# Kernel tuning notes

Measured on AMD Instinct MI355X. Metric: run time of the kernel, lower is better.

Reference implementation:

```python
import jax, jax.numpy as jnp
import numpy as np

D_MODEL = 2048
NUM_HEADS = 16
NUM_KV_HEADS = 4
HEAD_DIM = D_MODEL // NUM_HEADS
ROPE_THETA = 10000.0


def setup_inputs() -> dict:
    key = jax.random.key(0)
    ks = jax.random.split(key, 5)
    B, S = 2, 2048
    scale = 0.02
    return {
        "x": jax.random.normal(ks[0], (B, S, D_MODEL), dtype=jnp.float32),
        "wq": jax.random.normal(ks[1], (D_MODEL, NUM_HEADS * HEAD_DIM), dtype=jnp.float32) * scale,
        "wk": jax.random.normal(ks[2], (D_MODEL, NUM_KV_HEADS * HEAD_DIM), dtype=jnp.float32) * scale,
        "wv": jax.random.normal(ks[3], (D_MODEL, NUM_KV_HEADS * HEAD_DIM), dtype=jnp.float32) * scale,
        "wo": jax.random.normal(ks[4], (NUM_HEADS * HEAD_DIM, D_MODEL), dtype=jnp.float32) * scale,
    }


def _rope_cos_sin(seq_len, head_dim, dtype):
    # Llama-style: freqs over even indices, angles = pos * inv_freq
    inv_freq = 1.0 / (ROPE_THETA ** (jnp.arange(0, head_dim, 2, dtype=jnp.float32) / head_dim))
    ang = jnp.arange(seq_len, dtype=jnp.float32)[:, None] * inv_freq[None, :]  # [S, hd/2]
    cos = jnp.cos(ang).astype(dtype)[None, :, None, :]  # [1,S,1,hd/2]
    sin = jnp.sin(ang).astype(dtype)[None, :, None, :]
    return cos, sin


def _apply_rope(x, cos, sin):
    # x: [B,S,H,hd]; interleaved complex rotation on pairs (x[2i], x[2i+1])
    x1 = x[..., 0::2]
    x2 = x[..., 1::2]
    y1 = x1 * cos - x2 * sin
    y2 = x1 * sin + x2 * cos
    return jnp.stack([y1, y2], axis=-1).reshape(x.shape)


def reference(x, wq, wk, wv, wo):
    B, S, D = x.shape
    H, KV, hd = NUM_HEADS, NUM_KV_HEADS, HEAD_DIM
    g = H // KV
    q = (x @ wq).reshape(B, S, H, hd)
    k = (x @ wk).reshape(B, S, KV, hd)
    v = (x @ wv).reshape(B, S, KV, hd)
    cos, sin = _rope_cos_sin(S, hd, x.dtype)
    q = _apply_rope(q, cos, sin)
    k = _apply_rope(k, cos, sin)
    q = q.transpose(0, 2, 1, 3)  # [B,H,S,hd]
    k = k.transpose(0, 2, 1, 3)  # [B,KV,S,hd]
    v = v.transpose(0, 2, 1, 3)
    k = jnp.repeat(k, g, axis=1)  # GQA: [B,H,S,hd]
    v = jnp.repeat(v, g, axis=1)
    attn = jnp.einsum('bqsh,bqlh->bqsl', q, k) * (1.0 / np.sqrt(hd)).astype(np.float32)
    attn = jax.nn.softmax(attn, axis=-1)  # non-causal, as in source
    out = jnp.einsum('bqsl,bqlh->bqsh', attn, v)
    out = out.transpose(0, 2, 1, 3).reshape(B, S, D)
    return out @ wo
```

## Files before the change

### kernel.cpp

```cpp
#include <hip/hip_runtime.h>


typedef __attribute__((ext_vector_type(8))) short short8;
typedef __attribute__((ext_vector_type(4))) float f32x4;

#define DEV static __device__ __forceinline__

#define NB 2
#define NS 2048
#define ND 2048
#define NH 16
#define NKV 4
#define HD 128
#define NQKV 3072

DEV unsigned short f2bf(float f) {
  union { float f; unsigned u; } v; v.f = f;
  unsigned r = v.u + 0x7fffu + ((v.u >> 16) & 1u);
  return (unsigned short)(r >> 16);
}
DEV float bf2f(unsigned short u) {
  union { unsigned u; float f; } v; v.u = ((unsigned)u) << 16; return v.f;
}
DEV unsigned pack2bf_rne(float a, float b) {
  return (unsigned)f2bf(a) | ((unsigned)f2bf(b) << 16);
}
DEV unsigned cvtpk(float a, float b) {
  unsigned r;
  asm("v_cvt_pk_bf16_f32 %0, %1, %2" : "=v"(r) : "v"(a), "v"(b));
  return r;
}

DEV void swap32(unsigned &x, unsigned &y) {
  asm volatile("v_permlane32_swap_b32 %0, %1" : "+v"(x), "+v"(y));
}
DEV void swap16(unsigned &x, unsigned &y) {
  asm volatile("v_permlane16_swap_b32 %0, %1" : "+v"(x), "+v"(y));
}

typedef const __attribute__((address_space(1))) void* gas1_t;
typedef __attribute__((address_space(3))) void* las3_t;
DEV void gload16(const void* g, void* l) {
  __builtin_amdgcn_global_load_lds((gas1_t)g, (las3_t)l, 16, 0, 0);
}

DEV f32x4 mfma16(short8 a, short8 b, f32x4 c) {
  return __builtin_amdgcn_mfma_f32_16x16x32_bf16(a, b, c, 0, 0, 0);
}


__global__ __launch_bounds__(256) void convert_x_kernel(const float* __restrict__ x,
                                                        unsigned short* __restrict__ xb) {
  size_t i = ((size_t)blockIdx.x * 256 + threadIdx.x) * 4;
  float4 v = *(const float4*)(x + i);
  unsigned long long pack = (unsigned long long)f2bf(v.x)
                          | ((unsigned long long)f2bf(v.y) << 16)
                          | ((unsigned long long)f2bf(v.z) << 32)
                          | ((unsigned long long)f2bf(v.w) << 48);
  *(unsigned long long*)(xb + i) = pack;
}

__global__ __launch_bounds__(256) void transpose_w_kernel(const float* __restrict__ src,
                                                          unsigned short* __restrict__ dst,
                                                          int K, int N) {
  __shared__ float tile[64][65];
  const int k0 = blockIdx.x * 64, n0 = blockIdx.y * 64;
  for (int i = threadIdx.x; i < 1024; i += 256) {
    int r = i >> 4, c4 = (i & 15) * 4;
    float4 v = *(const float4*)&src[(size_t)(k0 + r) * N + n0 + c4];
    tile[r][c4] = v.x; tile[r][c4 + 1] = v.y; tile[r][c4 + 2] = v.z; tile[r][c4 + 3] = v.w;
  }
  __syncthreads();
  for (int i = threadIdx.x; i < 1024; i += 256) {
    int rn = i >> 4, k4 = (i & 15) * 4;
    ushort4 o;
    o.x = f2bf(tile[k4][rn]);     o.y = f2bf(tile[k4 + 1][rn]);
    o.z = f2bf(tile[k4 + 2][rn]); o.w = f2bf(tile[k4 + 3][rn]);
    *(ushort4*)&dst[(size_t)(n0 + rn) * K + k0 + k4] = o;
  }
}

__global__ __launch_bounds__(256) void rope_table_kernel(float2* __restrict__ tab) {
  int t = blockIdx.x * 256 + threadIdx.x;
  int s = t >> 6, i = t & 63;
  float freq = powf(10000.0f, -(float)i * (1.0f / 64.0f));
  float ang = (float)s * freq;
  tab[t] = make_float2(cosf(ang), sinf(ang));
}

__global__ __launch_bounds__(256) void rope_scatter_kernel(const unsigned short* __restrict__ QKV,
                                                           const float2* __restrict__ tab,
                                                           unsigned short* __restrict__ Qb,
                                                           unsigned short* __restrict__ Kb) {
  int t = blockIdx.x * 256 + threadIdx.x;
  const float qscale = 0.12751741161895452f;
  if (t < (1 << 22)) {
    int i = t & 63, h = (t >> 6) & 15, s = (t >> 10) & 2047, b = t >> 21;
    const unsigned short* p = QKV + (size_t)(b * NS + s) * NQKV + h * HD + 2 * i;
    float2 cs = tab[s * 64 + i];
    float x1 = bf2f(p[0]), x2 = bf2f(p[1]);
    unsigned short* q = Qb + (size_t)((b * NH + h) * NS + s) * HD + 2 * i;
    q[0] = f2bf((x1 * cs.x - x2 * cs.y) * qscale);
    q[1] = f2bf((x1 * cs.y + x2 * cs.x) * qscale);
  } else {
    int u = t - (1 << 22);
    int i = u & 63, kv = (u >> 6) & 3, s = (u >> 8) & 2047, b = u >> 19;
    const unsigned short* p = QKV + (size_t)(b * NS + s) * NQKV + 2048 + kv * HD + 2 * i;
    float2 cs = tab[s * 64 + i];
    float x1 = bf2f(p[0]), x2 = bf2f(p[1]);
    unsigned short* k = Kb + (size_t)((b * NKV + kv) * NS + s) * HD + 2 * i;
    k[0] = f2bf(x1 * cs.x - x2 * cs.y);
    k[1] = f2bf(x1 * cs.y + x2 * cs.x);
  }
}

__global__ __launch_bounds__(256) void transpose_v_kernel(const unsigned short* __restrict__ QKV,
                                                          unsigned short* __restrict__ Vt) {
  __shared__ unsigned short tile[64][65];
  const int bk = blockIdx.x, b = bk >> 2, kv = bk & 3;
  const int s0 = blockIdx.y * 64, d0 = blockIdx.z * 64;
  for (int i = threadIdx.x; i < 4096; i += 256) {
    int r = i >> 6, c = i & 63;
    tile[r][c] = QKV[(size_t)(b * NS + s0 + r) * NQKV + 2560 + kv * HD + d0 + c];
  }
  __syncthreads();
  for (int i = threadIdx.x; i < 4096; i += 256) {
    int r = i >> 6, c = i & 63;
    Vt[(size_t)((b * NKV + kv) * HD + d0 + r) * NS + s0 + c] = tile[c][r];
  }
}


template <int N, bool OUTBF16>
__global__ __launch_bounds__(512) void gemm256_kernel(const unsigned short* __restrict__ A,
                                                      const unsigned short* __restrict__ Bt,
                                                      void* __restrict__ Cout) {
  __shared__ unsigned short Sm[2][2][2][256 * 32];
  const int K = 2048, NT = K / 64;
  const int tid = threadIdx.x, wid = tid >> 6, lane = tid & 63;
  const int wm = wid >> 2, wn = wid & 3;

  const int nwg = gridDim.x * gridDim.y;
  const int bid = blockIdx.y * gridDim.x + blockIdx.x;
  const int swzb = (bid & 7) * (nwg >> 3) + (bid >> 3);
  const int m0 = (swzb % gridDim.x) * 256;
  const int n0 = (swzb / gridDim.x) * 256;

  const int cl = lane & 15, g = lane >> 4;
  const int rsw = (cl & 3) << 3;

  const int stg_row = tid >> 2;
  const int stg_colE = ((tid & 3) * 8) ^ ((stg_row & 3) << 3);
  const unsigned short* Abase = A + (size_t)(m0 + stg_row) * K + stg_colE;
  const unsigned short* Bbase = Bt + (size_t)(n0 + stg_row) * K + stg_colE;

  auto stage_half = [&](int buf, int kt, int h) {
    const int op = h & 1, kh = h >> 1;
    const unsigned short* s0 = (op ? Bbase : Abase) + kt + kh * 32;
    unsigned short* dst = &Sm[buf][op][kh][wid * 512];
    gload16(s0, dst);
    gload16(s0 + (size_t)128 * K, dst + 4096);
  };

  auto read_a = [&](int buf, int kh, int r) -> short8 {
    const int row = wm * 128 + r * 16 + cl;
    return *(const short8*)&Sm[buf][0][kh][row * 32 + ((g * 8) ^ rsw)];
  };
  auto read_b = [&](int buf, int kh, int cf) -> short8 {
    const int row = wn * 64 + cf * 16 + cl;
    return *(const short8*)&Sm[buf][1][kh][row * 32 + ((g * 8) ^ rsw)];
  };

  f32x4 acc[8][4] = {};
  short8 af[8];

#pragma unroll
  for (int h = 0; h < 4; ++h) stage_half(0, 0, h);

  for (int t = 0; t < NT - 1; ++t) {
    const int buf = t & 1, ktn = (t + 1) * 64;
#pragma unroll
    for (int ph = 0; ph < 4; ++ph) {
      stage_half(buf ^ 1, ktn, ph);
      asm volatile("s_waitcnt vmcnt(6)" ::: "memory");
      __builtin_amdgcn_s_barrier();
      const int kh = ph >> 1, ch = ph & 1;
      if (ch == 0) {
#pragma unroll
        for (int r = 0; r < 8; ++r) af[r] = read_a(buf, kh, r);
      }
      short8 b0 = read_b(buf, kh, ch * 2);
      short8 b1 = read_b(buf, kh, ch * 2 + 1);
      __builtin_amdgcn_s_setprio(1);
#pragma unroll
      for (int r = 0; r < 8; ++r) {
        acc[r][ch * 2]     = mfma16(af[r], b0, acc[r][ch * 2]);
        acc[r][ch * 2 + 1] = mfma16(af[r], b1, acc[r][ch * 2 + 1]);
      }
      __builtin_amdgcn_s_setprio(0);
      __builtin_amdgcn_s_barrier();
    }
  }

  asm volatile("s_waitcnt vmcnt(0)" ::: "memory");
  __builtin_amdgcn_s_barrier();
  {
    const int buf = (NT - 1) & 1;
#pragma unroll
    for (int kh = 0; kh < 2; ++kh) {
#pragma unroll
      for (int r = 0; r < 8; ++r) af[r] = read_a(buf, kh, r);
#pragma unroll
      for (int cf = 0; cf < 4; ++cf) {
        short8 b = read_b(buf, kh, cf);
#pragma unroll
        for (int r = 0; r < 8; ++r) acc[r][cf] = mfma16(af[r], b, acc[r][cf]);
      }
    }
  }

  if (OUTBF16) {
    unsigned short* C = (unsigned short*)Cout;
#pragma unroll
    for (int r = 0; r < 8; ++r) {
      const int row0 = m0 + wm * 128 + r * 16 + g * 4;
#pragma unroll
      for (int cf = 0; cf < 4; ++cf) {
        const int col = n0 + wn * 64 + cf * 16 + cl;
#pragma unroll
        for (int j = 0; j < 4; ++j)
          C[(size_t)(row0 + j) * N + col] = f2bf(acc[r][cf][j]);
      }
    }
  } else {
    float* C = (float*)Cout;
#pragma unroll
    for (int r = 0; r < 8; ++r) {
      const int row0 = m0 + wm * 128 + r * 16 + g * 4;
#pragma unroll
      for (int cf = 0; cf < 4; ++cf) {
        const int col = n0 + wn * 64 + cf * 16 + cl;
#pragma unroll
        for (int j = 0; j < 4; ++j)
          C[(size_t)(row0 + j) * N + col] = acc[r][cf][j];
      }
    }
  }
}


__global__ __launch_bounds__(256, 2) void attn_kernel(const unsigned short* __restrict__ Qb,
                                                      const unsigned short* __restrict__ Kb,
                                                      const unsigned short* __restrict__ Vt,
                                                      unsigned short* __restrict__ O) {
  __shared__ unsigned short Ks[2][64 * 128];
  __shared__ unsigned short Vs[2][128 * 64];
  const int tid = threadIdx.x, wid = tid >> 6, lane = tid & 63;
  const int blk = blockIdx.x;
  const int qt = blk & 15, h = (blk >> 4) & 15, b = blk >> 8;
  const int kvh = h >> 2;
  const int q0 = qt * 128 + wid * 32;

  const unsigned short* qhead = Qb + (size_t)((b * NH + h) * NS) * HD;
  const unsigned short* khead = Kb + (size_t)((b * NKV + kvh) * NS) * HD;
  const unsigned short* vhead = Vt + (size_t)((b * NKV + kvh) * HD) * NS;

  const int cl = lane & 15, g4 = (lane >> 4) * 4, hi8 = (lane >> 4) * 8;
  const int swk = (lane & 7) << 3;

  auto stageKV = [&](int buf, int kt) {
#pragma unroll
    for (int i = 0; i < 4; ++i) {
      int row = i * 16 + (tid >> 4);
      int col = ((tid & 15) * 8) ^ ((row & 7) << 3);
      gload16(khead + (size_t)(kt + row) * HD + col, &Ks[buf][i * 2048 + wid * 512]);
    }
#pragma unroll
    for (int i = 0; i < 4; ++i) {
      int row = i * 32 + (tid >> 3);
      int col = ((tid & 7) * 8) ^ ((row & 7) << 3);
      gload16(vhead + (size_t)row * NS + kt + col, &Vs[buf][i * 2048 + wid * 512]);
    }
  };

  stageKV(0, 0);

  short8 qf[2][4];
#pragma unroll
  for (int r = 0; r < 2; ++r)
#pragma unroll
    for (int kk = 0; kk < 4; ++kk)
      qf[r][kk] = *(const short8*)(qhead + (size_t)(q0 + r * 16 + cl) * HD + kk * 32 + hi8);

  f32x4 od[2][8] = {};
  float mrun[2] = {-1e30f, -1e30f}, lpart[2] = {0.f, 0.f};

  int cur = 0;
  for (int it = 0; it < NS / 64; ++it) {
    if (it + 1 < NS / 64) {
      stageKV(cur ^ 1, (it + 1) * 64);
      asm volatile("s_waitcnt vmcnt(8)" ::: "memory");
    } else {
      asm volatile("s_waitcnt vmcnt(0)" ::: "memory");
    }
    __builtin_amdgcn_s_barrier();

    const unsigned short* ks = Ks[cur];
    const unsigned short* vs = Vs[cur];

    f32x4 s[2][4];
#pragma unroll
    for (int r = 0; r < 2; ++r)
#pragma unroll
      for (int c4 = 0; c4 < 4; ++c4) s[r][c4] = f32x4{0.f, 0.f, 0.f, 0.f};
    __builtin_amdgcn_s_setprio(1);
#pragma unroll
    for (int c4 = 0; c4 < 4; ++c4)
#pragma unroll
      for (int kk = 0; kk < 4; ++kk) {
        short8 kf = *(const short8*)&ks[((c4 * 16 + cl) * 128 + kk * 32 + hi8) ^ swk];
        s[0][c4] = mfma16(kf, qf[0][kk], s[0][c4]);
        s[1][c4] = mfma16(kf, qf[1][kk], s[1][c4]);
      }
    __builtin_amdgcn_s_setprio(0);

    float mt[2];
#pragma unroll
    for (int r = 0; r < 2; ++r) {
      float m = fmaxf(fmaxf(fmaxf(s[r][0][0], s[r][0][1]), fmaxf(s[r][0][2], s[r][0][3])),
                      fmaxf(fmaxf(s[r][1][0], s[r][1][1]), fmaxf(s[r][1][2], s[r][1][3])));
      float m2 = fmaxf(fmaxf(fmaxf(s[r][2][0], s[r][2][1]), fmaxf(s[r][2][2], s[r][2][3])),
                       fmaxf(fmaxf(s[r][3][0], s[r][3][1]), fmaxf(s[r][3][2], s[r][3][3])));
      m = fmaxf(m, m2);
      m = fmaxf(m, __shfl_xor(m, 16, 64));
      m = fmaxf(m, __shfl_xor(m, 32, 64));
      mt[r] = m;
    }
    bool need = (mt[0] > mrun[0] + 8.0f) || (mt[1] > mrun[1] + 8.0f);
    if (__any(need)) {
#pragma unroll
      for (int r = 0; r < 2; ++r) {
        float mn = fmaxf(mrun[r], mt[r]);
        float corr = __builtin_amdgcn_exp2f(mrun[r] - mn);
        mrun[r] = mn;
        lpart[r] *= corr;
#pragma unroll
        for (int c = 0; c < 8; ++c)
          od[r][c] *= corr;
      }
    }
#pragma unroll
    for (int r = 0; r < 2; ++r) {
      float acc = 0.f;
#pragma unroll
      for (int c4 = 0; c4 < 4; ++c4)
#pragma unroll
        for (int j = 0; j < 4; ++j) {
          float p = __builtin_amdgcn_exp2f(s[r][c4][j] - mrun[r]);
          s[r][c4][j] = p;
          acc += p;
        }
      lpart[r] += acc;
    }

    short8 pb[2][2];
#pragma unroll
    for (int r = 0; r < 2; ++r) {
      unsigned w00 = cvtpk(s[r][0][0], s[r][0][1]), w01 = cvtpk(s[r][0][2], s[r][0][3]);
      unsigned w10 = cvtpk(s[r][1][0], s[r][1][1]), w11 = cvtpk(s[r][1][2], s[r][1][3]);
      unsigned w20 = cvtpk(s[r][2][0], s[r][2][1]), w21 = cvtpk(s[r][2][2], s[r][2][3]);
      unsigned w30 = cvtpk(s[r][3][0], s[r][3][1]), w31 = cvtpk(s[r][3][2], s[r][3][3]);
      union { unsigned u[4]; short8 v; } t0, t1;
      swap32(w00, w10); swap16(w00, w10); t0.u[0] = w00; t0.u[2] = w10;
      swap32(w01, w11); swap16(w01, w11); t0.u[1] = w01; t0.u[3] = w11;
      swap32(w20, w30); swap16(w20, w30); t1.u[0] = w20; t1.u[2] = w30;
      swap32(w21, w31); swap16(w21, w31); t1.u[1] = w21; t1.u[3] = w31;
      pb[r][0] = t0.v;
      pb[r][1] = t1.v;
    }

    __builtin_amdgcn_s_setprio(1);
#pragma unroll
    for (int c = 0; c < 8; ++c) {
      const int rr = c * 16 + cl;
      short8 vf0 = *(const short8*)&vs[(rr * 64 + hi8) ^ swk];
      short8 vf1 = *(const short8*)&vs[(rr * 64 + 32 + hi8) ^ swk];
      od[0][c] = mfma16(vf0, pb[0][0], od[0][c]);
      od[0][c] = mfma16(vf1, pb[0][1], od[0][c]);
      od[1][c] = mfma16(vf0, pb[1][0], od[1][c]);
      od[1][c] = mfma16(vf1, pb[1][1], od[1][c]);
    }
    __builtin_amdgcn_s_setprio(0);
    __builtin_amdgcn_s_barrier();
    cur ^= 1;
  }

  float linv[2];
#pragma unroll
  for (int r = 0; r < 2; ++r) {
    float l = lpart[r];
    l += __shfl_xor(l, 16, 64);
    l += __shfl_xor(l, 32, 64);
    linv[r] = 1.0f / l;
  }
#pragma unroll
  for (int r = 0; r < 2; ++r) {
    const size_t row = (size_t)(b * NS + q0 + 16 * r + cl);
#pragma unroll
    for (int c = 0; c < 8; ++c) {
      uint2 pk;
      pk.x = pack2bf_rne(od[r][c][0] * linv[r], od[r][c][1] * linv[r]);
      pk.y = pack2bf_rne(od[r][c][2] * linv[r], od[r][c][3] * linv[r]);
      *(uint2*)(O + row * ND + h * HD + c * 16 + g4) = pk;
    }
  }
}


extern "C" void kernel_launch(void* const* d_in, const int* in_sizes, int n_in,
                              void* d_out, int out_size, void* d_ws, size_t ws_size,
                              hipStream_t stream) {
  const float* x  = (const float*)d_in[0];
  const float* wq = (const float*)d_in[1];
  const float* wk = (const float*)d_in[2];
  const float* wv = (const float*)d_in[3];
  const float* wo = (const float*)d_in[4];
  float* out = (float*)d_out;
  char* ws = (char*)d_ws;

  unsigned short* xb   = (unsigned short*)(ws + 0);
  unsigned short* wT   = (unsigned short*)(ws + 16777216);
  unsigned short* woT  = (unsigned short*)(ws + 29360128);
  float2*         tab  = (float2*)(ws + 37748736);
  unsigned short* QKV  = (unsigned short*)(ws + 38797312);
  unsigned short* Qb   = xb;
  unsigned short* Kb   = wT;
  unsigned short* Vt   = (unsigned short*)(ws + 16777216 + 4194304);
  unsigned short* Obuf = QKV;

  convert_x_kernel<<<8192, 256, 0, stream>>>(x, xb);
  transpose_w_kernel<<<dim3(32, 32), 256, 0, stream>>>(wq, wT, 2048, 2048);
  transpose_w_kernel<<<dim3(32, 8),  256, 0, stream>>>(wk, wT + (size_t)2048 * 2048, 2048, 512);
  transpose_w_kernel<<<dim3(32, 8),  256, 0, stream>>>(wv, wT + (size_t)2560 * 2048, 2048, 512);
  transpose_w_kernel<<<dim3(32, 32), 256, 0, stream>>>(wo, woT, 2048, 2048);
  rope_table_kernel<<<512, 256, 0, stream>>>(tab);

  gemm256_kernel<NQKV, true><<<dim3(16, 12), 512, 0, stream>>>(xb, wT, QKV);

  rope_scatter_kernel<<<20480, 256, 0, stream>>>(QKV, tab, Qb, Kb);
  transpose_v_kernel<<<dim3(8, 32, 2), 256, 0, stream>>>(QKV, Vt);

  attn_kernel<<<512, 256, 0, stream>>>(Qb, Kb, Vt, Obuf);

  gemm256_kernel<ND, false><<<dim3(16, 8), 512, 0, stream>>>(Obuf, woT, out);
}
```

Baseline: 243.4 us.

## Fuse weight-prep launches and use 128-row tiles for output projection GEMM

The four weight-transpose launches and the rope-table launch are merged into one prep kernel that picks its work from blockIdx.y, which removes launch overhead and lets the small jobs run concurrently. The GEMM is templated on the M tile height. The output projection now uses BM=128, which doubles the grid from 128 to 256 workgroups so all CUs on the MI355X get work. The vmcnt waits are adjusted because the A operand now issues one load per stage instead of two. The smaller tiles lower per-block arithmetic intensity and increase redundant loads of B.

```diff
diff --git a/kernel.cpp b/kernel.cpp
--- a/kernel.cpp
+++ b/kernel.cpp
@@ -60,11 +60,31 @@
   *(unsigned long long*)(xb + i) = pack;
 }
 
-__global__ __launch_bounds__(256) void transpose_w_kernel(const float* __restrict__ src,
-                                                          unsigned short* __restrict__ dst,
-                                                          int K, int N) {
+__global__ __launch_bounds__(256) void prep_fused_kernel(const float* __restrict__ wq,
+                                                         const float* __restrict__ wk,
+                                                         const float* __restrict__ wv,
+                                                         const float* __restrict__ wo,
+                                                         unsigned short* __restrict__ wT,
+                                                         unsigned short* __restrict__ woT,
+                                                         float2* __restrict__ tab) {
+  const int ty = blockIdx.y;
+  if (ty >= 80) {
+    int t = ((ty - 80) * 32 + blockIdx.x) * 256 + threadIdx.x;
+    int s = t >> 6, i = t & 63;
+    float freq = powf(10000.0f, -(float)i * (1.0f / 64.0f));
+    float ang = (float)s * freq;
+    tab[t] = make_float2(cosf(ang), sinf(ang));
+    return;
+  }
+  const float* src;
+  unsigned short* dst;
+  int N, n0;
+  if (ty < 32)      { src = wq; dst = wT;                         N = 2048; n0 = ty * 64; }
+  else if (ty < 40) { src = wk; dst = wT + (size_t)2048 * 2048;   N = 512;  n0 = (ty - 32) * 64; }
+  else if (ty < 48) { src = wv; dst = wT + (size_t)2560 * 2048;   N = 512;  n0 = (ty - 40) * 64; }
+  else              { src = wo; dst = woT;                        N = 2048; n0 = (ty - 48) * 64; }
+  const int K = 2048, k0 = blockIdx.x * 64;
   __shared__ float tile[64][65];
-  const int k0 = blockIdx.x * 64, n0 = blockIdx.y * 64;
   for (int i = threadIdx.x; i < 1024; i += 256) {
     int r = i >> 4, c4 = (i & 15) * 4;
     float4 v = *(const float4*)&src[(size_t)(k0 + r) * N + n0 + c4];
@@ -78,14 +98,6 @@
     o.z = f2bf(tile[k4 + 2][rn]); o.w = f2bf(tile[k4 + 3][rn]);
     *(ushort4*)&dst[(size_t)(n0 + rn) * K + k0 + k4] = o;
   }
-}
-
-__global__ __launch_bounds__(256) void rope_table_kernel(float2* __restrict__ tab) {
-  int t = blockIdx.x * 256 + threadIdx.x;
-  int s = t >> 6, i = t & 63;
-  float freq = powf(10000.0f, -(float)i * (1.0f / 64.0f));
-  float ang = (float)s * freq;
-  tab[t] = make_float2(cosf(ang), sinf(ang));
 }
 
 __global__ __launch_bounds__(256) void rope_scatter_kernel(const unsigned short* __restrict__ QKV,
@@ -131,19 +143,21 @@
 }
 
 
-template <int N, bool OUTBF16>
+template <int N, int BM, bool OUTBF16>
 __global__ __launch_bounds__(512) void gemm256_kernel(const unsigned short* __restrict__ A,
                                                       const unsigned short* __restrict__ Bt,
                                                       void* __restrict__ Cout) {
-  __shared__ unsigned short Sm[2][2][2][256 * 32];
+  __shared__ unsigned short SmA[2][2][BM * 32];
+  __shared__ unsigned short SmB[2][2][256 * 32];
   const int K = 2048, NT = K / 64;
+  constexpr int RF = BM / 32;
   const int tid = threadIdx.x, wid = tid >> 6, lane = tid & 63;
   const int wm = wid >> 2, wn = wid & 3;
 
   const int nwg = gridDim.x * gridDim.y;
   const int bid = blockIdx.y * gridDim.x + blockIdx.x;
   const int swzb = (bid & 7) * (nwg >> 3) + (bid >> 3);
-  const int m0 = (swzb % gridDim.x) * 256;
+  const int m0 = (swzb % gridDim.x) * BM;
   const int n0 = (swzb / gridDim.x) * 256;
 
   const int cl = lane & 15, g = lane >> 4;
@@ -156,23 +170,30 @@
 
   auto stage_half = [&](int buf, int kt, int h) {
     const int op = h & 1, kh = h >> 1;
-    const unsigned short* s0 = (op ? Bbase : Abase) + kt + kh * 32;
-    unsigned short* dst = &Sm[buf][op][kh][wid * 512];
-    gload16(s0, dst);
-    gload16(s0 + (size_t)128 * K, dst + 4096);
+    if (op == 0) {
+      const unsigned short* s0 = Abase + kt + kh * 32;
+      unsigned short* dst = &SmA[buf][kh][wid * 512];
+      gload16(s0, dst);
+      if constexpr (BM == 256) gload16(s0 + (size_t)128 * K, dst + 4096);
+    } else {
+      const unsigned short* s0 = Bbase + kt + kh * 32;
+      unsigned short* dst = &SmB[buf][kh][wid * 512];
+      gload16(s0, dst);
+      gload16(s0 + (size_t)128 * K, dst + 4096);
+    }
   };
 
   auto read_a = [&](int buf, int kh, int r) -> short8 {
-    const int row = wm * 128 + r * 16 + cl;
-    return *(const short8*)&Sm[buf][0][kh][row * 32 + ((g * 8) ^ rsw)];
+    const int row = wm * (BM / 2) + r * 16 + cl;
+    return *(const short8*)&SmA[buf][kh][row * 32 + ((g * 8) ^ rsw)];
   };
   auto read_b = [&](int buf, int kh, int cf) -> short8 {
     const int row = wn * 64 + cf * 16 + cl;
-    return *(const short8*)&Sm[buf][1][kh][row * 32 + ((g * 8) ^ rsw)];
+    return *(const short8*)&SmB[buf][kh][row * 32 + ((g * 8) ^ rsw)];
   };
 
-  f32x4 acc[8][4] = {};
-  short8 af[8];
+  f32x4 acc[RF][4] = {};
+  short8 af[RF];
 
 #pragma unroll
   for (int h = 0; h < 4; ++h) stage_half(0, 0, h);
@@ -182,18 +203,23 @@
 #pragma unroll
     for (int ph = 0; ph < 4; ++ph) {
       stage_half(buf ^ 1, ktn, ph);
-      asm volatile("s_waitcnt vmcnt(6)" ::: "memory");
+      if constexpr (BM == 256) {
+        asm volatile("s_waitcnt vmcnt(6)" ::: "memory");
+      } else {
+        if (ph & 1) asm volatile("s_waitcnt vmcnt(6)" ::: "memory");
+        else        asm volatile("s_waitcnt vmcnt(4)" ::: "memory");
+      }
       __builtin_amdgcn_s_barrier();
       const int kh = ph >> 1, ch = ph & 1;
       if (ch == 0) {
 #pragma unroll
-        for (int r = 0; r < 8; ++r) af[r] = read_a(buf, kh, r);
+        for (int r = 0; r < RF; ++r) af[r] = read_a(buf, kh, r);
       }
       short8 b0 = read_b(buf, kh, ch * 2);
       short8 b1 = read_b(buf, kh, ch * 2 + 1);
       __builtin_amdgcn_s_setprio(1);
 #pragma unroll
-      for (int r = 0; r < 8; ++r) {
+      for (int r = 0; r < RF; ++r) {
         acc[r][ch * 2]     = mfma16(af[r], b0, acc[r][ch * 2]);
         acc[r][ch * 2 + 1] = mfma16(af[r], b1, acc[r][ch * 2 + 1]);
       }
@@ -209,12 +235,12 @@
 #pragma unroll
     for (int kh = 0; kh < 2; ++kh) {
 #pragma unroll
-      for (int r = 0; r < 8; ++r) af[r] = read_a(buf, kh, r);
+      for (int r = 0; r < RF; ++r) af[r] = read_a(buf, kh, r);
 #pragma unroll
       for (int cf = 0; cf < 4; ++cf) {
         short8 b = read_b(buf, kh, cf);
 #pragma unroll
-        for (int r = 0; r < 8; ++r) acc[r][cf] = mfma16(af[r], b, acc[r][cf]);
+        for (int r = 0; r < RF; ++r) acc[r][cf] = mfma16(af[r], b, acc[r][cf]);
       }
     }
   }
@@ -222,8 +248,8 @@
   if (OUTBF16) {
     unsigned short* C = (unsigned short*)Cout;
 #pragma unroll
-    for (int r = 0; r < 8; ++r) {
-      const int row0 = m0 + wm * 128 + r * 16 + g * 4;
+    for (int r = 0; r < RF; ++r) {
+      const int row0 = m0 + wm * (BM / 2) + r * 16 + g * 4;
 #pragma unroll
       for (int cf = 0; cf < 4; ++cf) {
         const int col = n0 + wn * 64 + cf * 16 + cl;
@@ -235,8 +261,8 @@
   } else {
     float* C = (float*)Cout;
 #pragma unroll
-    for (int r = 0; r < 8; ++r) {
-      const int row0 = m0 + wm * 128 + r * 16 + g * 4;
+    for (int r = 0; r < RF; ++r) {
+      const int row0 = m0 + wm * (BM / 2) + r * 16 + g * 4;
 #pragma unroll
       for (int cf = 0; cf < 4; ++cf) {
         const int col = n0 + wn * 64 + cf * 16 + cl;
@@ -439,18 +465,14 @@
   unsigned short* Obuf = QKV;
 
   convert_x_kernel<<<8192, 256, 0, stream>>>(x, xb);
-  transpose_w_kernel<<<dim3(32, 32), 256, 0, stream>>>(wq, wT, 2048, 2048);
-  transpose_w_kernel<<<dim3(32, 8),  256, 0, stream>>>(wk, wT + (size_t)2048 * 2048, 2048, 512);
-  transpose_w_kernel<<<dim3(32, 8),  256, 0, stream>>>(wv, wT + (size_t)2560 * 2048, 2048, 512);
-  transpose_w_kernel<<<dim3(32, 32), 256, 0, stream>>>(wo, woT, 2048, 2048);
-  rope_table_kernel<<<512, 256, 0, stream>>>(tab);
-
-  gemm256_kernel<NQKV, true><<<dim3(16, 12), 512, 0, stream>>>(xb, wT, QKV);
+  prep_fused_kernel<<<dim3(32, 96), 256, 0, stream>>>(wq, wk, wv, wo, wT, woT, tab);
+
+  gemm256_kernel<NQKV, 256, true><<<dim3(16, 12), 512, 0, stream>>>(xb, wT, QKV);
 
   rope_scatter_kernel<<<20480, 256, 0, stream>>>(QKV, tab, Qb, Kb);
   transpose_v_kernel<<<dim3(8, 32, 2), 256, 0, stream>>>(QKV, Vt);
 
   attn_kernel<<<512, 256, 0, stream>>>(Qb, Kb, Vt, Obuf);
 
-  gemm256_kernel<ND, false><<<dim3(16, 8), 512, 0, stream>>>(Obuf, woT, out);
-}
+  gemm256_kernel<ND, 128, false><<<dim3(32, 8), 512, 0, stream>>>(Obuf, woT, out);
+}
```

Result: slower. 263.3 us (+8.1%).

## Fuse prep kernels, scatter QKV in GEMM epilogue, load V directly in attention

Applied to the files above, without the earlier changes.

Merges the four weight transposes and the rope table into one launch. The QKV GEMM epilogue now writes Q and K straight into head-major layout and V pre-transposed, so the separate scatter and V-transpose passes go away. RoPE is applied in place with 16-byte vector loads and stores. The attention kernel stops staging V through LDS and reads V fragments from global memory into registers each iteration, which adds register pressure and uncoalesced global reads in exchange for less LDS use and a barrier-free pipeline.

```diff
diff --git a/kernel.cpp b/kernel.cpp
--- a/kernel.cpp
+++ b/kernel.cpp
@@ -60,11 +60,31 @@
   *(unsigned long long*)(xb + i) = pack;
 }
 
-__global__ __launch_bounds__(256) void transpose_w_kernel(const float* __restrict__ src,
-                                                          unsigned short* __restrict__ dst,
-                                                          int K, int N) {
+__global__ __launch_bounds__(256) void prep_fused_kernel(const float* __restrict__ wq,
+                                                         const float* __restrict__ wk,
+                                                         const float* __restrict__ wv,
+                                                         const float* __restrict__ wo,
+                                                         unsigned short* __restrict__ wT,
+                                                         unsigned short* __restrict__ woT,
+                                                         float2* __restrict__ tab) {
+  const int ty = blockIdx.y;
+  if (ty >= 80) {
+    int t = ((ty - 80) * 32 + blockIdx.x) * 256 + threadIdx.x;
+    int s = t >> 6, i = t & 63;
+    float freq = powf(10000.0f, -(float)i * (1.0f / 64.0f));
+    float ang = (float)s * freq;
+    tab[t] = make_float2(cosf(ang), sinf(ang));
+    return;
+  }
+  const float* src;
+  unsigned short* dst;
+  int N, n0;
+  if (ty < 32)      { src = wq; dst = wT;                         N = 2048; n0 = ty * 64; }
+  else if (ty < 40) { src = wk; dst = wT + (size_t)2048 * 2048;   N = 512;  n0 = (ty - 32) * 64; }
+  else if (ty < 48) { src = wv; dst = wT + (size_t)2560 * 2048;   N = 512;  n0 = (ty - 40) * 64; }
+  else              { src = wo; dst = woT;                        N = 2048; n0 = (ty - 48) * 64; }
+  const int K = 2048, k0 = blockIdx.x * 64;
   __shared__ float tile[64][65];
-  const int k0 = blockIdx.x * 64, n0 = blockIdx.y * 64;
   for (int i = threadIdx.x; i < 1024; i += 256) {
     int r = i >> 4, c4 = (i & 15) * 4;
     float4 v = *(const float4*)&src[(size_t)(k0 + r) * N + n0 + c4];
@@ -80,62 +100,42 @@
   }
 }
 
-__global__ __launch_bounds__(256) void rope_table_kernel(float2* __restrict__ tab) {
-  int t = blockIdx.x * 256 + threadIdx.x;
-  int s = t >> 6, i = t & 63;
-  float freq = powf(10000.0f, -(float)i * (1.0f / 64.0f));
-  float ang = (float)s * freq;
-  tab[t] = make_float2(cosf(ang), sinf(ang));
-}
-
-__global__ __launch_bounds__(256) void rope_scatter_kernel(const unsigned short* __restrict__ QKV,
-                                                           const float2* __restrict__ tab,
-                                                           unsigned short* __restrict__ Qb,
-                                                           unsigned short* __restrict__ Kb) {
+__global__ __launch_bounds__(256) void rope_inplace_kernel(unsigned short* __restrict__ Qb,
+                                                           unsigned short* __restrict__ Kb,
+                                                           const float2* __restrict__ tab) {
   int t = blockIdx.x * 256 + threadIdx.x;
   const float qscale = 0.12751741161895452f;
-  if (t < (1 << 22)) {
-    int i = t & 63, h = (t >> 6) & 15, s = (t >> 10) & 2047, b = t >> 21;
-    const unsigned short* p = QKV + (size_t)(b * NS + s) * NQKV + h * HD + 2 * i;
-    float2 cs = tab[s * 64 + i];
-    float x1 = bf2f(p[0]), x2 = bf2f(p[1]);
-    unsigned short* q = Qb + (size_t)((b * NH + h) * NS + s) * HD + 2 * i;
-    q[0] = f2bf((x1 * cs.x - x2 * cs.y) * qscale);
-    q[1] = f2bf((x1 * cs.y + x2 * cs.x) * qscale);
-  } else {
-    int u = t - (1 << 22);
-    int i = u & 63, kv = (u >> 6) & 3, s = (u >> 8) & 2047, b = u >> 19;
-    const unsigned short* p = QKV + (size_t)(b * NS + s) * NQKV + 2048 + kv * HD + 2 * i;
-    float2 cs = tab[s * 64 + i];
-    float x1 = bf2f(p[0]), x2 = bf2f(p[1]);
-    unsigned short* k = Kb + (size_t)((b * NKV + kv) * NS + s) * HD + 2 * i;
-    k[0] = f2bf(x1 * cs.x - x2 * cs.y);
-    k[1] = f2bf(x1 * cs.y + x2 * cs.x);
-  }
-}
-
-__global__ __launch_bounds__(256) void transpose_v_kernel(const unsigned short* __restrict__ QKV,
-                                                          unsigned short* __restrict__ Vt) {
-  __shared__ unsigned short tile[64][65];
-  const int bk = blockIdx.x, b = bk >> 2, kv = bk & 3;
-  const int s0 = blockIdx.y * 64, d0 = blockIdx.z * 64;
-  for (int i = threadIdx.x; i < 4096; i += 256) {
-    int r = i >> 6, c = i & 63;
-    tile[r][c] = QKV[(size_t)(b * NS + s0 + r) * NQKV + 2560 + kv * HD + d0 + c];
-  }
-  __syncthreads();
-  for (int i = threadIdx.x; i < 4096; i += 256) {
-    int r = i >> 6, c = i & 63;
-    Vt[(size_t)((b * NKV + kv) * HD + d0 + r) * NS + s0 + c] = tile[c][r];
-  }
-}
-
-
-template <int N, bool OUTBF16>
+  const bool isQ = t < (1 << 20);
+  unsigned short* base = isQ ? Qb : Kb;
+  int u = isQ ? t : t - (1 << 20);
+  const int i8 = u & 15, s = (u >> 4) & 2047, bh = u >> 15;
+  unsigned short* p = base + ((size_t)bh * NS + s) * HD + i8 * 8;
+  short8 v = *(short8*)p;
+  const unsigned short* vu = (const unsigned short*)&v;
+  const float2* tp = tab + s * 64 + i8 * 4;
+  unsigned short o[8];
+#pragma unroll
+  for (int w = 0; w < 4; ++w) {
+    float x1 = bf2f(vu[2 * w]), x2 = bf2f(vu[2 * w + 1]);
+    float2 cs = tp[w];
+    float y1 = x1 * cs.x - x2 * cs.y;
+    float y2 = x1 * cs.y + x2 * cs.x;
+    if (isQ) { y1 *= qscale; y2 *= qscale; }
+    o[2 * w] = f2bf(y1); o[2 * w + 1] = f2bf(y2);
+  }
+  *(short8*)p = *(const short8*)o;
+}
+
+
+template <int N, int MODE>
 __global__ __launch_bounds__(512) void gemm256_kernel(const unsigned short* __restrict__ A,
                                                       const unsigned short* __restrict__ Bt,
-                                                      void* __restrict__ Cout) {
-  __shared__ unsigned short Sm[2][2][2][256 * 32];
+                                                      void* __restrict__ Cout,
+                                                      unsigned short* __restrict__ Qb,
+                                                      unsigned short* __restrict__ Kb,
+                                                      unsigned short* __restrict__ Vt) {
+  __shared__ unsigned short SmA[2][2][256 * 32];
+  __shared__ unsigned short SmB[2][2][256 * 32];
   const int K = 2048, NT = K / 64;
   const int tid = threadIdx.x, wid = tid >> 6, lane = tid & 63;
   const int wm = wid >> 2, wn = wid & 3;
@@ -157,18 +157,18 @@
   auto stage_half = [&](int buf, int kt, int h) {
     const int op = h & 1, kh = h >> 1;
     const unsigned short* s0 = (op ? Bbase : Abase) + kt + kh * 32;
-    unsigned short* dst = &Sm[buf][op][kh][wid * 512];
+    unsigned short* dst = op ? &SmB[buf][kh][wid * 512] : &SmA[buf][kh][wid * 512];
     gload16(s0, dst);
     gload16(s0 + (size_t)128 * K, dst + 4096);
   };
 
   auto read_a = [&](int buf, int kh, int r) -> short8 {
     const int row = wm * 128 + r * 16 + cl;
-    return *(const short8*)&Sm[buf][0][kh][row * 32 + ((g * 8) ^ rsw)];
+    return *(const short8*)&SmA[buf][kh][row * 32 + ((g * 8) ^ rsw)];
   };
   auto read_b = [&](int buf, int kh, int cf) -> short8 {
     const int row = wn * 64 + cf * 16 + cl;
-    return *(const short8*)&Sm[buf][1][kh][row * 32 + ((g * 8) ^ rsw)];
+    return *(const short8*)&SmB[buf][kh][row * 32 + ((g * 8) ^ rsw)];
   };
 
   f32x4 acc[8][4] = {};
@@ -219,8 +219,8 @@
     }
   }
 
-  if (OUTBF16) {
-    unsigned short* C = (unsigned short*)Cout;
+  if constexpr (MODE == 0) {
+    float* C = (float*)Cout;
 #pragma unroll
     for (int r = 0; r < 8; ++r) {
       const int row0 = m0 + wm * 128 + r * 16 + g * 4;
@@ -229,20 +229,41 @@
         const int col = n0 + wn * 64 + cf * 16 + cl;
 #pragma unroll
         for (int j = 0; j < 4; ++j)
-          C[(size_t)(row0 + j) * N + col] = f2bf(acc[r][cf][j]);
+          C[(size_t)(row0 + j) * N + col] = acc[r][cf][j];
       }
     }
   } else {
-    float* C = (float*)Cout;
+    const int colbase = n0 + wn * 64;
 #pragma unroll
     for (int r = 0; r < 8; ++r) {
       const int row0 = m0 + wm * 128 + r * 16 + g * 4;
-#pragma unroll
-      for (int cf = 0; cf < 4; ++cf) {
-        const int col = n0 + wn * 64 + cf * 16 + cl;
-#pragma unroll
-        for (int j = 0; j < 4; ++j)
-          C[(size_t)(row0 + j) * N + col] = acc[r][cf][j];
+      const int bb = row0 >> 11, ss = row0 & (NS - 1);
+      if (colbase < 2048) {
+        const int h = colbase >> 7, dl = colbase & 127;
+#pragma unroll
+        for (int cf = 0; cf < 4; ++cf) {
+          unsigned short* dst = Qb + ((size_t)(bb * NH + h) * NS + ss) * HD + dl + cf * 16 + cl;
+#pragma unroll
+          for (int j = 0; j < 4; ++j) dst[(size_t)j * HD] = f2bf(acc[r][cf][j]);
+        }
+      } else if (colbase < 2560) {
+        const int kv = (colbase - 2048) >> 7, dl = (colbase - 2048) & 127;
+#pragma unroll
+        for (int cf = 0; cf < 4; ++cf) {
+          unsigned short* dst = Kb + ((size_t)(bb * NKV + kv) * NS + ss) * HD + dl + cf * 16 + cl;
+#pragma unroll
+          for (int j = 0; j < 4; ++j) dst[(size_t)j * HD] = f2bf(acc[r][cf][j]);
+        }
+      } else {
+        const int kv = (colbase - 2560) >> 7, dl = (colbase - 2560) & 127;
+#pragma unroll
+        for (int cf = 0; cf < 4; ++cf) {
+          const int d = dl + cf * 16 + cl;
+          uint2 pk2;
+          pk2.x = pack2bf_rne(acc[r][cf][0], acc[r][cf][1]);
+          pk2.y = pack2bf_rne(acc[r][cf][2], acc[r][cf][3]);
+          *(uint2*)(Vt + ((size_t)(bb * NKV + kv) * HD + d) * NS + ss) = pk2;
+        }
       }
     }
   }
@@ -254,7 +275,6 @@
                                                       const unsigned short* __restrict__ Vt,
                                                       unsigned short* __restrict__ O) {
   __shared__ unsigned short Ks[2][64 * 128];
-  __shared__ unsigned short Vs[2][128 * 64];
   const int tid = threadIdx.x, wid = tid >> 6, lane = tid & 63;
   const int blk = blockIdx.x;
   const int qt = blk & 15, h = (blk >> 4) & 15, b = blk >> 8;
@@ -268,22 +288,16 @@
   const int cl = lane & 15, g4 = (lane >> 4) * 4, hi8 = (lane >> 4) * 8;
   const int swk = (lane & 7) << 3;
 
-  auto stageKV = [&](int buf, int kt) {
+  auto stageK = [&](int buf, int kt) {
 #pragma unroll
     for (int i = 0; i < 4; ++i) {
       int row = i * 16 + (tid >> 4);
       int col = ((tid & 15) * 8) ^ ((row & 7) << 3);
       gload16(khead + (size_t)(kt + row) * HD + col, &Ks[buf][i * 2048 + wid * 512]);
     }
-#pragma unroll
-    for (int i = 0; i < 4; ++i) {
-      int row = i * 32 + (tid >> 3);
-      int col = ((tid & 7) * 8) ^ ((row & 7) << 3);
-      gload16(vhead + (size_t)row * NS + kt + col, &Vs[buf][i * 2048 + wid * 512]);
-    }
   };
 
-  stageKV(0, 0);
+  stageK(0, 0);
 
   short8 qf[2][4];
 #pragma unroll
@@ -297,16 +311,19 @@
 
   int cur = 0;
   for (int it = 0; it < NS / 64; ++it) {
-    if (it + 1 < NS / 64) {
-      stageKV(cur ^ 1, (it + 1) * 64);
-      asm volatile("s_waitcnt vmcnt(8)" ::: "memory");
-    } else {
-      asm volatile("s_waitcnt vmcnt(0)" ::: "memory");
-    }
-    __builtin_amdgcn_s_barrier();
+    const int kt = it * 64;
+    __syncthreads();
+
+    short8 vfa[8], vfb[8];
+#pragma unroll
+    for (int c = 0; c < 8; ++c) {
+      const unsigned short* vrow = vhead + (size_t)(c * 16 + cl) * NS + kt + hi8;
+      vfa[c] = *(const short8*)(vrow);
+      vfb[c] = *(const short8*)(vrow + 32);
+    }
+    if (it + 1 < NS / 64) stageK(cur ^ 1, kt + 64);
 
     const unsigned short* ks = Ks[cur];
-    const unsigned short* vs = Vs[cur];
 
     f32x4 s[2][4];
 #pragma unroll
@@ -382,16 +399,12 @@
     __builtin_amdgcn_s_setprio(1);
 #pragma unroll
     for (int c = 0; c < 8; ++c) {
-      const int rr = c * 16 + cl;
-      short8 vf0 = *(const short8*)&vs[(rr * 64 + hi8) ^ swk];
-      short8 vf1 = *(const short8*)&vs[(rr * 64 + 32 + hi8) ^ swk];
-      od[0][c] = mfma16(vf0, pb[0][0], od[0][c]);
-      od[0][c] = mfma16(vf1, pb[0][1], od[0][c]);
-      od[1][c] = mfma16(vf0, pb[1][0], od[1][c]);
-      od[1][c] = mfma16(vf1, pb[1][1], od[1][c]);
+      od[0][c] = mfma16(vfa[c], pb[0][0], od[0][c]);
+      od[0][c] = mfma16(vfb[c], pb[0][1], od[0][c]);
+      od[1][c] = mfma16(vfa[c], pb[1][0], od[1][c]);
+      od[1][c] = mfma16(vfb[c], pb[1][1], od[1][c]);
     }
     __builtin_amdgcn_s_setprio(0);
-    __builtin_amdgcn_s_barrier();
     cur ^= 1;
   }
 
@@ -432,25 +445,19 @@
   unsigned short* wT   = (unsigned short*)(ws + 16777216);
   unsigned short* woT  = (unsigned short*)(ws + 29360128);
   float2*         tab  = (float2*)(ws + 37748736);
-  unsigned short* QKV  = (unsigned short*)(ws + 38797312);
-  unsigned short* Qb   = xb;
-  unsigned short* Kb   = wT;
-  unsigned short* Vt   = (unsigned short*)(ws + 16777216 + 4194304);
-  unsigned short* Obuf = QKV;
+  unsigned short* Qb   = (unsigned short*)(ws + 38797312);
+  unsigned short* Kb   = (unsigned short*)(ws + 55574528);
+  unsigned short* Vt   = (unsigned short*)(ws + 59768832);
+  unsigned short* Obuf = xb;
 
   convert_x_kernel<<<8192, 256, 0, stream>>>(x, xb);
-  transpose_w_kernel<<<dim3(32, 32), 256, 0, stream>>>(wq, wT, 2048, 2048);
-  transpose_w_kernel<<<dim3(32, 8),  256, 0, stream>>>(wk, wT + (size_t)2048 * 2048, 2048, 512);
-  transpose_w_kernel<<<dim3(32, 8),  256, 0, stream>>>(wv, wT + (size_t)2560 * 2048, 2048, 512);
-  transpose_w_kernel<<<dim3(32, 32), 256, 0, stream>>>(wo, woT, 2048, 2048);
-  rope_table_kernel<<<512, 256, 0, stream>>>(tab);
-
-  gemm256_kernel<NQKV, true><<<dim3(16, 12), 512, 0, stream>>>(xb, wT, QKV);
-
-  rope_scatter_kernel<<<20480, 256, 0, stream>>>(QKV, tab, Qb, Kb);
-  transpose_v_kernel<<<dim3(8, 32, 2), 256, 0, stream>>>(QKV, Vt);
+  prep_fused_kernel<<<dim3(32, 96), 256, 0, stream>>>(wq, wk, wv, wo, wT, woT, tab);
+
+  gemm256_kernel<NQKV, 1><<<dim3(16, 12), 512, 0, stream>>>(xb, wT, nullptr, Qb, Kb, Vt);
+
+  rope_inplace_kernel<<<5120, 256, 0, stream>>>(Qb, Kb, tab);
 
   attn_kernel<<<512, 256, 0, stream>>>(Qb, Kb, Vt, Obuf);
 
-  gemm256_kernel<ND, false><<<dim3(16, 8), 512, 0, stream>>>(Obuf, woT, out);
-}
+  gemm256_kernel<ND, 0><<<dim3(16, 8), 512, 0, stream>>>(Obuf, woT, out, nullptr, nullptr, nullptr);
+}
```

Result: slower. 344.9 us (+41.7%).
